# Kernel optimization log

Measured on AMD Instinct MI355X. Metric: run time of the kernel, lower is better.

Reference implementation:

```python
import jax, jax.numpy as jnp
import numpy as np
from jax import lax


def setup_inputs() -> dict:
    key = jax.random.key(0)
    kx, kih, khh, kb = jax.random.split(key, 4)
    B, T, I, H = 32, 512, 1024, 1024
    s_ih = 1.0 / np.sqrt(I)
    s_hh = 1.0 / np.sqrt(H)
    return {
        "x": jax.random.normal(kx, (B, T, I), dtype=jnp.float32),
        "W_ih": jax.random.normal(kih, (4 * H, I), dtype=jnp.float32) * s_ih,
        "W_hh": jax.random.normal(khh, (4 * H, H), dtype=jnp.float32) * s_hh,
        "b": jax.random.normal(kb, (4 * H,), dtype=jnp.float32) * s_hh,
    }


def reference(x, W_ih, W_hh, b):
    # x: [B, T, I]; LSTM with gate order i, f, g, o (equinox LSTMCell).
    B, T, I = x.shape
    H = W_hh.shape[1]
    # Precompute the input projection for all timesteps (same math, hoisted).
    xW = jnp.einsum("bti,gi->btg", x, W_ih) + b  # [B, T, 4H]
    xW_t = jnp.transpose(xW, (1, 0, 2))          # [T, B, 4H]

    h0 = jnp.zeros((B, H), dtype=x.dtype)
    c0 = jnp.zeros((B, H), dtype=x.dtype)

    def step(carry, xt):
        h, c = carry
        z = xt + h @ W_hh.T                      # [B, 4H]
        i, f, g, o = jnp.split(z, 4, axis=-1)
        i = jax.nn.sigmoid(i)
        f = jax.nn.sigmoid(f)
        g = jnp.tanh(g)
        o = jax.nn.sigmoid(o)
        c = f * c + i * g
        h = o * jnp.tanh(c)
        return (h, c), h

    _, hs = lax.scan(step, (h0, c0), xW_t)       # hs: [T, B, H]
    return jnp.transpose(hs, (1, 0, 2))          # [B, T, H]
```

## Files before the change

kernel.cpp:

```cpp
#include <hip/hip_runtime.h>
#include <stdint.h>

#define BB 32
#define TT 512
#define KK 1024
#define GG 4096
#define MM 16384
#define SCAN_WGS 64
#define HPAD 1032

typedef __attribute__((ext_vector_type(8))) short short8;
typedef __attribute__((ext_vector_type(4))) short short4v;
typedef __attribute__((ext_vector_type(4))) float f32x4;
typedef unsigned long long u64;

__device__ inline short f2bf(float f) {
  union { float f; unsigned u; } v; v.f = f;
  unsigned r = (v.u + 0x7FFFu + ((v.u >> 16) & 1u)) >> 16;
  return (short)(unsigned short)r;
}
__device__ inline float bf2f(short s) {
  union { unsigned u; float f; } v; v.u = ((unsigned)(unsigned short)s) << 16;
  return v.f;
}
__device__ inline float sigmoid_f(float x) { return 1.0f / (1.0f + __expf(-x)); }
__device__ inline float tanh_f(float x)    { return 1.0f - 2.0f / (__expf(2.0f * x) + 1.0f); }


__global__ void zero_ws(unsigned* __restrict__ p, int n) {
  int i = blockIdx.x * 256 + threadIdx.x;
  if (i < n) p[i] = 0u;
}

__global__ void cvt_bf16(const float* __restrict__ in, short* __restrict__ out, int n4) {
  int i = blockIdx.x * 256 + threadIdx.x;
  if (i >= n4) return;
  f32x4 v = *(const f32x4*)(in + (size_t)i * 4);
  short4v o;
  o.x = f2bf(v.x); o.y = f2bf(v.y); o.z = f2bf(v.z); o.w = f2bf(v.w);
  *(short4v*)(out + (size_t)i * 4) = o;
}

__global__ void pack_whh(const float* __restrict__ Whh, short* __restrict__ wpack) {
  int idx = blockIdx.x * 256 + threadIdx.x;
  if (idx >= SCAN_WGS * 8 * 16 * 64) return;
  int lane = idx & 63;
  int s    = (idx >> 6) & 15;
  int wv   = (idx >> 10) & 7;
  int wg   = idx >> 13;
  int g    = wv >> 1, kh = wv & 1;
  int row  = g * 1024 + wg * 16 + (lane & 15);
  int k    = kh * 512 + s * 32 + (lane >> 4) * 8;
  const float* src = Whh + (size_t)row * KK + k;
  short8 v;
#pragma unroll
  for (int j = 0; j < 8; ++j) v[j] = f2bf(src[j]);
  *(short8*)(wpack + ((size_t)((wg * 8 + wv) * 16 + s)) * 512 + lane * 8) = v;
}

template <bool XWF32>
__global__ __launch_bounds__(256) void gemm_xw(const short* __restrict__ A,
                                               const short* __restrict__ Bw,
                                               const float* __restrict__ bias,
                                               void* __restrict__ Cv) {
  __shared__ short As[128 * 32];
  __shared__ short Bs[128 * 32];
  const int tid = threadIdx.x;
  const int m0 = blockIdx.y * 128;
  const int n0 = blockIdx.x * 128;
  const int lane = tid & 63, wv = tid >> 6;
  const int wm = (wv >> 1) * 64, wn = (wv & 1) * 64;
  const int fr = lane & 15;
  const int fq = (lane >> 4) * 8;
  const int quad = lane >> 4;
  f32x4 acc[4][4];
#pragma unroll
  for (int i = 0; i < 4; ++i)
#pragma unroll
    for (int j = 0; j < 4; ++j) acc[i][j] = (f32x4){0.f, 0.f, 0.f, 0.f};

  const int sr = tid >> 2;
  const int sc = (tid & 3) * 8;
  const short* Ag = A + (size_t)(m0 + sr) * KK + sc;
  const short* Bg = Bw + (size_t)(n0 + sr) * KK + sc;

  for (int kb = 0; kb < KK; kb += 32) {
    short8 a0 = *(const short8*)(Ag + kb);
    short8 a1 = *(const short8*)(Ag + (size_t)64 * KK + kb);
    short8 b0 = *(const short8*)(Bg + kb);
    short8 b1 = *(const short8*)(Bg + (size_t)64 * KK + kb);
    __syncthreads();
    *(short8*)&As[sr * 32 + sc] = a0;
    *(short8*)&As[(64 + sr) * 32 + sc] = a1;
    *(short8*)&Bs[sr * 32 + sc] = b0;
    *(short8*)&Bs[(64 + sr) * 32 + sc] = b1;
    __syncthreads();
    short8 af[4], bf[4];
#pragma unroll
    for (int i = 0; i < 4; ++i) {
      af[i] = *(const short8*)&As[(wm + i * 16 + fr) * 32 + fq];
      bf[i] = *(const short8*)&Bs[(wn + i * 16 + fr) * 32 + fq];
    }
#pragma unroll
    for (int i = 0; i < 4; ++i)
#pragma unroll
      for (int j = 0; j < 4; ++j)
        acc[i][j] = __builtin_amdgcn_mfma_f32_16x16x32_bf16(af[i], bf[j], acc[i][j], 0, 0, 0);
  }
#pragma unroll
  for (int i = 0; i < 4; ++i) {
    int mrow = m0 + wm + i * 16 + quad * 4;
#pragma unroll
    for (int j = 0; j < 4; ++j) {
      int ncol = n0 + wn + j * 16 + fr;
      float bv = bias[ncol];
#pragma unroll
      for (int r = 0; r < 4; ++r) {
        float v = acc[i][j][r] + bv;
        size_t idx = (size_t)(mrow + r) * GG + ncol;
        if (XWF32) ((float*)Cv)[idx] = v;
        else       ((short*)Cv)[idx] = f2bf(v);
      }
    }
  }
}

template <bool XWF32>
__global__ __launch_bounds__(512) void lstm_scan(const void* __restrict__ xWv,
                                                 const short* __restrict__ wpack,
                                                 short* __restrict__ hbuf,
                                                 float* __restrict__ out,
                                                 unsigned* __restrict__ arr) {
  const int wg = blockIdx.x;
  const int tid = threadIdx.x;
  const int lane = tid & 63;
  const int wv = tid >> 6;
  const int kh = wv & 1;
  const int abrow = lane & 15;
  const int quad = lane >> 4;

  short8 wreg[16];
  {
    const short* wp = wpack + ((size_t)((wg * 8 + wv) * 16)) * 512 + lane * 8;
#pragma unroll
    for (int s = 0; s < 16; ++s) wreg[s] = *(const short8*)(wp + s * 512);
  }

  __shared__ short hstage[32 * HPAD];
  __shared__ float partials[8 * 2 * 64 * 4];

  const int gb = tid >> 4, gj = tid & 15;
  const int jglob = wg * 16 + gj;
  const int gmt = gb >> 4, grow = gb & 15;
  const int gquad = grow >> 2, gr = grow & 3;
  const int gl = (gquad << 4) | gj;
  float c_reg = 0.f;

  const float* xwf = (const float*)xWv;
  const short* xwh = (const short*)xWv;

  const int lbase0 = abrow * HPAD + kh * 512 + quad * 8;
  const int lbase1 = (abrow + 16) * HPAD + kh * 512 + quad * 8;

  float xwv_[4];
#pragma unroll
  for (int g = 0; g < 4; ++g) {
    size_t xi = ((size_t)gb * TT) * GG + (size_t)g * 1024 + jglob;
    xwv_[g] = XWF32 ? xwf[xi] : bf2f(xwh[xi]);
  }

  int cur = 0;
#pragma unroll 1
  for (int t = 0; t < TT; ++t) {
    const u64* hb64 = (const u64*)(hbuf + cur * (BB * KK));
    u64 hv[16];
#pragma unroll
    for (int it = 0; it < 16; ++it) {
      int c = it * 512 + tid;
      hv[it] = __hip_atomic_load(&hb64[c], __ATOMIC_RELAXED,
                                 __HIP_MEMORY_SCOPE_AGENT);
    }
    float xwn[4];
    if (t + 1 < TT) {
#pragma unroll
      for (int g = 0; g < 4; ++g) {
        size_t xi = ((size_t)(gb * TT + t + 1)) * GG + (size_t)g * 1024 + jglob;
        xwn[g] = XWF32 ? xwf[xi] : bf2f(xwh[xi]);
      }
    }
#pragma unroll
    for (int it = 0; it < 16; ++it) {
      int c = it * 512 + tid;
      int row = c >> 8, col8 = c & 255;
      *(u64*)&hstage[row * HPAD + col8 * 4] = hv[it];
    }
    __syncthreads();

    f32x4 acc0 = (f32x4){0.f, 0.f, 0.f, 0.f};
    f32x4 acc1 = (f32x4){0.f, 0.f, 0.f, 0.f};
#pragma unroll
    for (int s = 0; s < 16; ++s) {
      short8 a0 = *(const short8*)&hstage[lbase0 + s * 32];
      short8 a1 = *(const short8*)&hstage[lbase1 + s * 32];
      acc0 = __builtin_amdgcn_mfma_f32_16x16x32_bf16(a0, wreg[s], acc0, 0, 0, 0);
      acc1 = __builtin_amdgcn_mfma_f32_16x16x32_bf16(a1, wreg[s], acc1, 0, 0, 0);
    }
    *(f32x4*)&partials[((wv * 2 + 0) * 64 + lane) * 4] = acc0;
    *(f32x4*)&partials[((wv * 2 + 1) * 64 + lane) * 4] = acc1;
    __syncthreads();

    float z[4];
#pragma unroll
    for (int g = 0; g < 4; ++g) {
      z[g] = partials[(((g * 2 + 0) * 2 + gmt) * 64 + gl) * 4 + gr] +
             partials[(((g * 2 + 1) * 2 + gmt) * 64 + gl) * 4 + gr] + xwv_[g];
    }
    float i_ = sigmoid_f(z[0]);
    float f_ = sigmoid_f(z[1]);
    float g_ = tanh_f(z[2]);
    float o_ = sigmoid_f(z[3]);
    c_reg = f_ * c_reg + i_ * g_;
    float h_ = o_ * tanh_f(c_reg);
    out[((size_t)gb * TT + t) * 1024 + jglob] = h_;

    unsigned hb16 = (unsigned)(unsigned short)f2bf(h_);
    unsigned oth = __shfl_xor(hb16, 1, 64);
    if (!(gj & 1)) {
      unsigned packed = hb16 | (oth << 16);
      unsigned* dst = (unsigned*)(hbuf + (cur ^ 1) * (BB * KK) + gb * KK + jglob);
      __hip_atomic_store(dst, packed, __ATOMIC_RELAXED, __HIP_MEMORY_SCOPE_AGENT);
    }

    if (t + 1 < TT) {
      __syncthreads();
      if (tid < 64) {
        unsigned tgt = (unsigned)(t + 1);
        if (tid == 0)
          __hip_atomic_store(&arr[(size_t)wg * 16], tgt, __ATOMIC_RELAXED,
                             __HIP_MEMORY_SCOPE_AGENT);
        unsigned a = 0;
        while (true) {
          if (a < tgt)
            a = __hip_atomic_load(&arr[(size_t)tid * 16], __ATOMIC_RELAXED,
                                  __HIP_MEMORY_SCOPE_AGENT);
          if (__all(a >= tgt)) break;
          __builtin_amdgcn_s_sleep(1);
        }
      }
      __syncthreads();
    }
#pragma unroll
    for (int g = 0; g < 4; ++g) xwv_[g] = xwn[g];
    cur ^= 1;
  }
}


extern "C" void kernel_launch(void* const* d_in, const int* in_sizes, int n_in,
                              void* d_out, int out_size, void* d_ws, size_t ws_size,
                              hipStream_t stream) {
  const float* x    = (const float*)d_in[0];
  const float* Wih  = (const float*)d_in[1];
  const float* Whh  = (const float*)d_in[2];
  const float* bias = (const float*)d_in[3];
  float* out = (float*)d_out;

  char* ws = (char*)d_ws;
  const size_t o_xbf   = 0;
  const size_t o_wih   = 33554432;
  const size_t o_wpack = 41943040;
  const size_t o_hbuf  = 50331648;
  const size_t o_bar   = 50462720;
  const size_t o_xw    = 50466816;
  const bool xwf32 = ws_size >= (o_xw + (size_t)MM * GG * 4);

  short* xbf    = (short*)(ws + o_xbf);
  short* wihbf  = (short*)(ws + o_wih);
  short* wpack  = (short*)(ws + o_wpack);
  short* hbuf   = (short*)(ws + o_hbuf);
  unsigned* arr = (unsigned*)(ws + o_bar);
  void* xw      = (void*)(ws + o_xw);

  zero_ws<<<(33792 + 255) / 256, 256, 0, stream>>>((unsigned*)(ws + o_hbuf), 33792);
  cvt_bf16<<<16384, 256, 0, stream>>>(x, xbf, 4194304);
  cvt_bf16<<<4096, 256, 0, stream>>>(Wih, wihbf, 1048576);
  pack_whh<<<2048, 256, 0, stream>>>(Whh, wpack);

  dim3 g1(GG / 128, MM / 128);
  if (xwf32) gemm_xw<true ><<<g1, 256, 0, stream>>>(xbf, wihbf, bias, xw);
  else       gemm_xw<false><<<g1, 256, 0, stream>>>(xbf, wihbf, bias, xw);

  if (xwf32) lstm_scan<true ><<<SCAN_WGS, 512, 0, stream>>>(xw, wpack, hbuf, out, arr);
  else       lstm_scan<false><<<SCAN_WGS, 512, 0, stream>>>(xw, wpack, hbuf, out, arr);
}
```

Baseline: 2.436 ms.

## Replace global barrier with per-element timestep-tagged h handoff and batch-split scan

The scan kernel drops the all-workgroup arrival barrier. Each h value is now stored as a 32-bit word carrying its bf16 value plus a timestep tag, and consumers spin only on stale words. Workgroups are split into two batch groups of 16 rows, each group with 32 hidden slices. Each wave owns all four gates for 4 hidden units over the full K, so the cross-wave partial-sum LDS reduction and its extra syncthreads disappear and gate math runs directly on the MFMA accumulator. The cost is double the h storage and traffic (32-bit tagged words), twice the weight registers per lane, and a polling loop that relies on relaxed-atomic visibility of the tags.

```diff
diff --git a/kernel.cpp b/kernel.cpp
--- a/kernel.cpp
+++ b/kernel.cpp
@@ -6,6 +6,7 @@
 #define KK 1024
 #define GG 4096
 #define MM 16384
+#define NSLICE 32
 #define SCAN_WGS 64
 #define HPAD 1032
 
@@ -43,19 +44,19 @@
 
 __global__ void pack_whh(const float* __restrict__ Whh, short* __restrict__ wpack) {
   int idx = blockIdx.x * 256 + threadIdx.x;
-  if (idx >= SCAN_WGS * 8 * 16 * 64) return;
-  int lane = idx & 63;
-  int s    = (idx >> 6) & 15;
-  int wv   = (idx >> 10) & 7;
-  int wg   = idx >> 13;
-  int g    = wv >> 1, kh = wv & 1;
-  int row  = g * 1024 + wg * 16 + (lane & 15);
-  int k    = kh * 512 + s * 32 + (lane >> 4) * 8;
+  if (idx >= NSLICE * 8 * 32 * 64) return;
+  int lane  = idx & 63;
+  int s     = (idx >> 6) & 31;
+  int nt    = (idx >> 11) & 7;
+  int slice = idx >> 14;
+  int c     = lane & 15;
+  int row   = (c & 3) * 1024 + slice * 32 + nt * 4 + (c >> 2);
+  int k     = s * 32 + (lane >> 4) * 8;
   const float* src = Whh + (size_t)row * KK + k;
   short8 v;
 #pragma unroll
   for (int j = 0; j < 8; ++j) v[j] = f2bf(src[j]);
-  *(short8*)(wpack + ((size_t)((wg * 8 + wv) * 16 + s)) * 512 + lane * 8) = v;
+  *(short8*)(wpack + ((size_t)((slice * 8 + nt) * 32 + s)) * 512 + lane * 8) = v;
 }
 
 template <bool XWF32>
@@ -128,130 +129,108 @@
 template <bool XWF32>
 __global__ __launch_bounds__(512) void lstm_scan(const void* __restrict__ xWv,
                                                  const short* __restrict__ wpack,
-                                                 short* __restrict__ hbuf,
-                                                 float* __restrict__ out,
-                                                 unsigned* __restrict__ arr) {
+                                                 unsigned* __restrict__ hbuf,
+                                                 float* __restrict__ out) {
   const int wg = blockIdx.x;
+  const int group = wg >> 5;
+  const int slice = wg & 31;
   const int tid = threadIdx.x;
   const int lane = tid & 63;
   const int wv = tid >> 6;
-  const int kh = wv & 1;
-  const int abrow = lane & 15;
   const int quad = lane >> 4;
-
-  short8 wreg[16];
+  const int bloc = lane & 15;
+  const int bglob = group * 16 + bloc;
+  const int jglob = slice * 32 + wv * 4 + quad;
+
+  short8 wreg[32];
   {
-    const short* wp = wpack + ((size_t)((wg * 8 + wv) * 16)) * 512 + lane * 8;
-#pragma unroll
-    for (int s = 0; s < 16; ++s) wreg[s] = *(const short8*)(wp + s * 512);
-  }
-
-  __shared__ short hstage[32 * HPAD];
-  __shared__ float partials[8 * 2 * 64 * 4];
-
-  const int gb = tid >> 4, gj = tid & 15;
-  const int jglob = wg * 16 + gj;
-  const int gmt = gb >> 4, grow = gb & 15;
-  const int gquad = grow >> 2, gr = grow & 3;
-  const int gl = (gquad << 4) | gj;
+    const short* wp = wpack + ((size_t)((slice * 8 + wv) * 32)) * 512 + lane * 8;
+#pragma unroll
+    for (int s = 0; s < 32; ++s) wreg[s] = *(const short8*)(wp + (size_t)s * 512);
+  }
+
+  __shared__ short hstage[2][16 * HPAD];
+
   float c_reg = 0.f;
-
   const float* xwf = (const float*)xWv;
   const short* xwh = (const short*)xWv;
 
-  const int lbase0 = abrow * HPAD + kh * 512 + quad * 8;
-  const int lbase1 = (abrow + 16) * HPAD + kh * 512 + quad * 8;
-
   float xwv_[4];
-#pragma unroll
-  for (int g = 0; g < 4; ++g) {
-    size_t xi = ((size_t)gb * TT) * GG + (size_t)g * 1024 + jglob;
-    xwv_[g] = XWF32 ? xwf[xi] : bf2f(xwh[xi]);
-  }
-
-  int cur = 0;
+  {
+    size_t xb = ((size_t)bglob * TT) * GG + jglob;
+#pragma unroll
+    for (int g = 0; g < 4; ++g)
+      xwv_[g] = XWF32 ? xwf[xb + (size_t)g * 1024] : bf2f(xwh[xb + (size_t)g * 1024]);
+  }
+
 #pragma unroll 1
   for (int t = 0; t < TT; ++t) {
-    const u64* hb64 = (const u64*)(hbuf + cur * (BB * KK));
+    const int buf = t & 1;
+    u64* hb = (u64*)hbuf + (size_t)buf * 16384 + (size_t)group * 8192;
     u64 hv[16];
 #pragma unroll
-    for (int it = 0; it < 16; ++it) {
-      int c = it * 512 + tid;
-      hv[it] = __hip_atomic_load(&hb64[c], __ATOMIC_RELAXED,
-                                 __HIP_MEMORY_SCOPE_AGENT);
-    }
-    float xwn[4];
+    for (int i = 0; i < 16; ++i)
+      hv[i] = __hip_atomic_load(&hb[i * 512 + tid], __ATOMIC_RELAXED,
+                                __HIP_MEMORY_SCOPE_AGENT);
+    float xwn[4] = {0.f, 0.f, 0.f, 0.f};
     if (t + 1 < TT) {
-#pragma unroll
-      for (int g = 0; g < 4; ++g) {
-        size_t xi = ((size_t)(gb * TT + t + 1)) * GG + (size_t)g * 1024 + jglob;
-        xwn[g] = XWF32 ? xwf[xi] : bf2f(xwh[xi]);
+      size_t xb = ((size_t)bglob * TT + t + 1) * GG + jglob;
+#pragma unroll
+      for (int g = 0; g < 4; ++g)
+        xwn[g] = XWF32 ? xwf[xb + (size_t)g * 1024] : bf2f(xwh[xb + (size_t)g * 1024]);
+    }
+    const unsigned tagexp = (unsigned)t;
+    unsigned stale = 0u;
+#pragma unroll
+    for (int i = 0; i < 16; ++i) {
+      unsigned t0 = ((unsigned)(hv[i] >> 16)) & 0xffffu;
+      unsigned t1 = (unsigned)(hv[i] >> 48);
+      if (t0 != tagexp || t1 != tagexp) stale |= (1u << i);
+    }
+    while (stale) {
+#pragma unroll
+      for (int i = 0; i < 16; ++i) {
+        if (stale & (1u << i)) {
+          u64 v = __hip_atomic_load(&hb[i * 512 + tid], __ATOMIC_RELAXED,
+                                    __HIP_MEMORY_SCOPE_AGENT);
+          unsigned t0 = ((unsigned)(v >> 16)) & 0xffffu;
+          unsigned t1 = (unsigned)(v >> 48);
+          if (t0 == tagexp && t1 == tagexp) { hv[i] = v; stale &= ~(1u << i); }
+        }
       }
-    }
-#pragma unroll
-    for (int it = 0; it < 16; ++it) {
-      int c = it * 512 + tid;
-      int row = c >> 8, col8 = c & 255;
-      *(u64*)&hstage[row * HPAD + col8 * 4] = hv[it];
+      if (stale) __builtin_amdgcn_s_sleep(1);
+    }
+    short* hs = hstage[buf];
+#pragma unroll
+    for (int i = 0; i < 16; ++i) {
+      unsigned lo = (unsigned)hv[i] & 0xffffu;
+      unsigned hi = ((unsigned)(hv[i] >> 32)) & 0xffffu;
+      *(unsigned*)&hs[i * HPAD + 2 * tid] = lo | (hi << 16);
     }
     __syncthreads();
 
-    f32x4 acc0 = (f32x4){0.f, 0.f, 0.f, 0.f};
-    f32x4 acc1 = (f32x4){0.f, 0.f, 0.f, 0.f};
-#pragma unroll
-    for (int s = 0; s < 16; ++s) {
-      short8 a0 = *(const short8*)&hstage[lbase0 + s * 32];
-      short8 a1 = *(const short8*)&hstage[lbase1 + s * 32];
-      acc0 = __builtin_amdgcn_mfma_f32_16x16x32_bf16(a0, wreg[s], acc0, 0, 0, 0);
-      acc1 = __builtin_amdgcn_mfma_f32_16x16x32_bf16(a1, wreg[s], acc1, 0, 0, 0);
-    }
-    *(f32x4*)&partials[((wv * 2 + 0) * 64 + lane) * 4] = acc0;
-    *(f32x4*)&partials[((wv * 2 + 1) * 64 + lane) * 4] = acc1;
-    __syncthreads();
-
-    float z[4];
-#pragma unroll
-    for (int g = 0; g < 4; ++g) {
-      z[g] = partials[(((g * 2 + 0) * 2 + gmt) * 64 + gl) * 4 + gr] +
-             partials[(((g * 2 + 1) * 2 + gmt) * 64 + gl) * 4 + gr] + xwv_[g];
-    }
-    float i_ = sigmoid_f(z[0]);
-    float f_ = sigmoid_f(z[1]);
-    float g_ = tanh_f(z[2]);
-    float o_ = sigmoid_f(z[3]);
+    f32x4 acc = (f32x4){0.f, 0.f, 0.f, 0.f};
+    const short* hrow = hs + bloc * HPAD + quad * 8;
+#pragma unroll
+    for (int s = 0; s < 32; ++s) {
+      short8 b = *(const short8*)(hrow + s * 32);
+      acc = __builtin_amdgcn_mfma_f32_16x16x32_bf16(wreg[s], b, acc, 0, 0, 0);
+    }
+
+    float i_ = sigmoid_f(acc[0] + xwv_[0]);
+    float f_ = sigmoid_f(acc[1] + xwv_[1]);
+    float g_ = tanh_f(acc[2] + xwv_[2]);
+    float o_ = sigmoid_f(acc[3] + xwv_[3]);
     c_reg = f_ * c_reg + i_ * g_;
     float h_ = o_ * tanh_f(c_reg);
-    out[((size_t)gb * TT + t) * 1024 + jglob] = h_;
-
-    unsigned hb16 = (unsigned)(unsigned short)f2bf(h_);
-    unsigned oth = __shfl_xor(hb16, 1, 64);
-    if (!(gj & 1)) {
-      unsigned packed = hb16 | (oth << 16);
-      unsigned* dst = (unsigned*)(hbuf + (cur ^ 1) * (BB * KK) + gb * KK + jglob);
-      __hip_atomic_store(dst, packed, __ATOMIC_RELAXED, __HIP_MEMORY_SCOPE_AGENT);
-    }
-
-    if (t + 1 < TT) {
-      __syncthreads();
-      if (tid < 64) {
-        unsigned tgt = (unsigned)(t + 1);
-        if (tid == 0)
-          __hip_atomic_store(&arr[(size_t)wg * 16], tgt, __ATOMIC_RELAXED,
-                             __HIP_MEMORY_SCOPE_AGENT);
-        unsigned a = 0;
-        while (true) {
-          if (a < tgt)
-            a = __hip_atomic_load(&arr[(size_t)tid * 16], __ATOMIC_RELAXED,
-                                  __HIP_MEMORY_SCOPE_AGENT);
-          if (__all(a >= tgt)) break;
-          __builtin_amdgcn_s_sleep(1);
-        }
-      }
-      __syncthreads();
-    }
+    out[((size_t)bglob * TT + t) * 1024 + jglob] = h_;
+
+    unsigned hw = ((unsigned)(t + 1) << 16) | (unsigned)(unsigned short)f2bf(h_);
+    __hip_atomic_store(&hbuf[(size_t)(buf ^ 1) * 32768 + (size_t)bglob * 1024 + jglob],
+                       hw, __ATOMIC_RELAXED, __HIP_MEMORY_SCOPE_AGENT);
+
 #pragma unroll
     for (int g = 0; g < 4; ++g) xwv_[g] = xwn[g];
-    cur ^= 1;
   }
 }
 
@@ -270,18 +249,16 @@
   const size_t o_wih   = 33554432;
   const size_t o_wpack = 41943040;
   const size_t o_hbuf  = 50331648;
-  const size_t o_bar   = 50462720;
-  const size_t o_xw    = 50466816;
+  const size_t o_xw    = 50593792;
   const bool xwf32 = ws_size >= (o_xw + (size_t)MM * GG * 4);
 
-  short* xbf    = (short*)(ws + o_xbf);
-  short* wihbf  = (short*)(ws + o_wih);
-  short* wpack  = (short*)(ws + o_wpack);
-  short* hbuf   = (short*)(ws + o_hbuf);
-  unsigned* arr = (unsigned*)(ws + o_bar);
-  void* xw      = (void*)(ws + o_xw);
-
-  zero_ws<<<(33792 + 255) / 256, 256, 0, stream>>>((unsigned*)(ws + o_hbuf), 33792);
+  short* xbf      = (short*)(ws + o_xbf);
+  short* wihbf    = (short*)(ws + o_wih);
+  short* wpack    = (short*)(ws + o_wpack);
+  unsigned* hbuf  = (unsigned*)(ws + o_hbuf);
+  void* xw        = (void*)(ws + o_xw);
+
+  zero_ws<<<256, 256, 0, stream>>>(hbuf, 65536);
   cvt_bf16<<<16384, 256, 0, stream>>>(x, xbf, 4194304);
   cvt_bf16<<<4096, 256, 0, stream>>>(Wih, wihbf, 1048576);
   pack_whh<<<2048, 256, 0, stream>>>(Whh, wpack);
@@ -290,6 +267,6 @@
   if (xwf32) gemm_xw<true ><<<g1, 256, 0, stream>>>(xbf, wihbf, bias, xw);
   else       gemm_xw<false><<<g1, 256, 0, stream>>>(xbf, wihbf, bias, xw);
 
-  if (xwf32) lstm_scan<true ><<<SCAN_WGS, 512, 0, stream>>>(xw, wpack, hbuf, out, arr);
-  else       lstm_scan<false><<<SCAN_WGS, 512, 0, stream>>>(xw, wpack, hbuf, out, arr);
-}
+  if (xwf32) lstm_scan<true ><<<SCAN_WGS, 512, 0, stream>>>(xw, wpack, hbuf, out);
+  else       lstm_scan<false><<<SCAN_WGS, 512, 0, stream>>>(xw, wpack, hbuf, out);
+}
```

Measured after the change: 5.048 ms. 107% more time.
